# Kernel optimization log

Hardware: AMD Instinct MI355X
Metric: run time of the kernel (lower is better)

Reference implementation:

```python
import jax, jax.numpy as jnp
import numpy as np

K_REP = 4          # repulsion neighbors
REP_THRESH = 0.02  # repulsion distance threshold
K_NORM = 16        # PCA-normal neighborhood size (includes self)
CD_W, REP_W, NORM_W = 1.0, 0.1, 0.01


def _pdist2(x, y):
    # squared pairwise distances: [B,N,M]
    xx = (x * x).sum(-1)
    yy = (y * y).sum(-1)
    return xx[..., :, None] + yy[..., None, :] - 2.0 * jnp.einsum('bnd,bmd->bnm', x, y)


def _gather_points(pts, idx):
    # pts: [B,N,3], idx: [B,N,k] -> [B,N,k,3]
    return jax.vmap(lambda p, i: p[i])(pts, idx)


def _pca_normals(pts):
    # normals via PCA over K_NORM nearest neighbors (self included)
    D = _pdist2(pts, pts)                       # [B,N,N]
    _, idx = jax.lax.top_k(-D, K_NORM)          # [B,N,K]
    nb = _gather_points(pts, idx)               # [B,N,K,3]
    c = nb - nb.mean(axis=-2, keepdims=True)
    cov = jnp.einsum('bnkd,bnke->bnde', c, c) / K_NORM  # [B,N,3,3]
    _, vecs = jnp.linalg.eigh(cov)              # ascending eigenvalues
    return vecs[..., :, 0]                      # eigenvector of smallest eigenvalue


def reference(pred, gt):
    # --- chamfer distance (squared, bidirectional mean) ---
    Dpg = _pdist2(pred, gt)                     # [B,N,M]
    cd = Dpg.min(axis=-1).mean() + Dpg.min(axis=-2).mean()

    # --- repulsion loss: k=4 NN on pred (excluding self) ---
    Dpp = _pdist2(pred, pred)                   # [B,N,N]
    neg_d2, _ = jax.lax.top_k(-Dpp, K_REP + 1)  # nearest incl. self
    d2 = -neg_d2[..., 1:]                       # drop self
    d = jnp.sqrt(jnp.maximum(d2, 1e-12))
    rep = jax.nn.relu(REP_THRESH - d).mean()

    # --- normal consistency via PCA normals (k=16) ---
    n_pred = _pca_normals(pred)
    n_gt = _pca_normals(gt)
    normc = 1.0 - (n_pred * n_gt).sum(-1).mean()

    return CD_W * cd + REP_W * rep + NORM_W * normc


def setup_inputs() -> dict:
    key = jax.random.key(0)
    k1, k2 = jax.random.split(key)
    B, N = 8, 2048
    pred = jax.random.uniform(k1, (B, N, 3), dtype=jnp.float32)
    gt = jax.random.uniform(k2, (B, N, 3), dtype=jnp.float32)
    return {"pred": pred, "gt": gt}
```

## Files before the change

kernel.cpp:

```cpp
#include <hip/hip_runtime.h>


#define NB 8
#define NP 2048
#define KW 10
#define KN 16


__device__ __forceinline__ float f_slapy2(float x, float y) {
    float xa = fabsf(x), ya = fabsf(y);
    float w = fmaxf(xa, ya), zm = fminf(xa, ya);
    if (zm == 0.f) return w;
    float q = zm / w;
    return w * sqrtf(1.f + q * q);
}

__device__ __forceinline__ void f_slartg(float f, float g, float* cs, float* sn, float* r) {
    if (g == 0.f) { *cs = 1.f; *sn = 0.f; *r = f; }
    else if (f == 0.f) { *cs = 0.f; *sn = copysignf(1.f, g); *r = fabsf(g); }
    else {
        float d = sqrtf(__fadd_rn(__fmul_rn(f, f), __fmul_rn(g, g)));
        *cs = fabsf(f) / d;
        *r  = copysignf(d, f);
        *sn = g / *r;
    }
}

__device__ void f_slaev2(float a, float b, float c,
                         float* rt1, float* rt2, float* cs1, float* sn1) {
    float sm = a + c;
    float df = a - c;
    float adf = fabsf(df);
    float tb = b + b;
    float ab = fabsf(tb);
    float acmx, acmn;
    if (fabsf(a) > fabsf(c)) { acmx = a; acmn = c; } else { acmx = c; acmn = a; }
    float rt;
    if (adf > ab)      { float q = ab / adf; rt = adf * sqrtf(1.f + q * q); }
    else if (adf < ab) { float q = adf / ab; rt = ab * sqrtf(1.f + q * q); }
    else               rt = ab * sqrtf(2.f);
    int sgn1;
    if (sm < 0.f) {
        *rt1 = 0.5f * (sm - rt); sgn1 = -1;
        *rt2 = (acmx / *rt1) * acmn - (b / *rt1) * b;
    } else if (sm > 0.f) {
        *rt1 = 0.5f * (sm + rt); sgn1 = 1;
        *rt2 = (acmx / *rt1) * acmn - (b / *rt1) * b;
    } else {
        *rt1 = 0.5f * rt; *rt2 = -0.5f * rt; sgn1 = 1;
    }
    float cs; int sgn2;
    if (df >= 0.f) { cs = df + rt; sgn2 = 1; }
    else           { cs = df - rt; sgn2 = -1; }
    float acs = fabsf(cs);
    if (acs > ab) {
        float ct = -tb / cs;
        *sn1 = 1.f / sqrtf(1.f + ct * ct);
        *cs1 = ct * *sn1;
    } else {
        if (ab == 0.f) { *cs1 = 1.f; *sn1 = 0.f; }
        else {
            float tn = -cs / tb;
            *cs1 = 1.f / sqrtf(1.f + tn * tn);
            *sn1 = tn * *cs1;
        }
    }
    if (sgn1 == sgn2) { float tn = *cs1; *cs1 = -*sn1; *sn1 = tn; }
}


__device__ __forceinline__ float get3(float a, float b, float c, int i) {
    return i == 0 ? a : (i == 1 ? b : c);
}
__device__ __forceinline__ void set3(float& a, float& b, float& c, int i, float v) {
    a = (i == 0) ? v : a;
    b = (i == 1) ? v : b;
    c = (i == 2) ? v : c;
}
__device__ __forceinline__ float get2(float a, float b, int i) { return i == 0 ? a : b; }
__device__ __forceinline__ void set2(float& a, float& b, int i, float v) {
    a = (i == 0) ? v : a;
    b = (i == 1) ? v : b;
}

#define DGET(i)    get3(dd0, dd1, dd2, (i))
#define DSET(i, v) set3(dd0, dd1, dd2, (i), (v))
#define EGET(i)    get2(ee0, ee1, (i))
#define ESET(i, v) set2(ee0, ee1, (i), (v))
#define ZGET(r, c)    get3(z##r##0, z##r##1, z##r##2, (c))
#define ZSET(r, c, v) set3(z##r##0, z##r##1, z##r##2, (c), (v))
#define ZROT(r, ca, cb, cc, ss) { float zt_ = ZGET(r, (ca)); float zb_ = ZGET(r, (cb)); \
    ZSET(r, (ca), (cc) * zt_ - (ss) * zb_); ZSET(r, (cb), (ss) * zt_ + (cc) * zb_); }
#define ZROT3(ca, cb, cc, ss) { ZROT(0, (ca), (cb), (cc), (ss)) ZROT(1, (ca), (cb), (cc), (ss)) ZROT(2, (ca), (cb), (cc), (ss)) }

__device__ void ssyevd3_evec0(float a00, float a10, float a20,
                              float a11, float a21, float a22,
                              float* ox, float* oy, float* oz) {
    float dd0, dd1, dd2, ee0, ee1;
    float tau = 0.f, v2 = 0.f;
    float xnorm = fabsf(a20);
    if (xnorm == 0.f) {
        tau = 0.f;
        dd0 = a00; dd1 = a11; dd2 = a22; ee0 = a10; ee1 = a21;
    } else {
        float beta = -copysignf(f_slapy2(a10, xnorm), a10);
        tau = (beta - a10) / beta;
        float inv = 1.f / (a10 - beta);
        v2 = a20 * inv;
        float x1 = tau * (a11 + a21 * v2);
        float x2 = tau * (a21 + a22 * v2);
        float alpha = -0.5f * tau * (x1 + x2 * v2);
        float w1 = x1 + alpha;
        float w2 = x2 + alpha * v2;
        float b11 = a11 - 2.f * w1;
        float b21 = a21 - v2 * w1 - w2;
        float b22 = a22 - 2.f * (v2 * w2);
        dd0 = a00; dd1 = b11; dd2 = b22; ee0 = beta; ee1 = b21;
    }
    const float eps    = 5.9604645e-08f;
    const float eps2   = eps * eps;
    const float safmin = 1.1754944e-38f;
    const float ssfmax = sqrtf(1.f / safmin) / 3.f;
    const float ssfmin = sqrtf(safmin) / eps2;
    const int n = 3, nmaxit = 90;
    float z00 = 1.f, z01 = 0.f, z02 = 0.f;
    float z10 = 0.f, z11 = 1.f, z12 = 0.f;
    float z20 = 0.f, z21 = 0.f, z22 = 1.f;
    int jtot = 0;
    int l1 = 1;

    while (true) {
        if (l1 > n) break;
        if (l1 > 1) ESET(l1 - 2, 0.f);
        int m = n;
        {
            bool found = false;
            #pragma unroll
            for (int mi = 1; mi <= 2; ++mi) {
                if (!found && mi >= l1) {
                    float tst = fabsf(EGET(mi - 1));
                    if (tst == 0.f) { m = mi; found = true; }
                    else if (tst <= (sqrtf(fabsf(DGET(mi - 1))) * sqrtf(fabsf(DGET(mi)))) * eps) {
                        ESET(mi - 1, 0.f); m = mi; found = true;
                    }
                }
            }
        }
        int l = l1, lsv = l, lend = m, lendsv = lend;
        l1 = m + 1;
        if (lend == l) continue;

        float anorm = 0.f;
        #pragma unroll
        for (int i = 1; i <= 3; ++i)
            if (i >= l && i <= lend) anorm = fmaxf(anorm, fabsf(DGET(i - 1)));
        #pragma unroll
        for (int i = 1; i <= 2; ++i)
            if (i >= l && i <= lend - 1) anorm = fmaxf(anorm, fabsf(EGET(i - 1)));
        int iscale = 0; float sclto = 1.f;
        if (anorm == 0.f) continue;
        if (anorm > ssfmax) { iscale = 1; sclto = ssfmax; }
        else if (anorm < ssfmin) { iscale = 2; sclto = ssfmin; }
        if (iscale) {
            float mul = sclto / anorm;
            #pragma unroll
            for (int i = 1; i <= 3; ++i)
                if (i >= l && i <= lend) DSET(i - 1, DGET(i - 1) * mul);
            #pragma unroll
            for (int i = 1; i <= 2; ++i)
                if (i >= l && i <= lend - 1) ESET(i - 1, EGET(i - 1) * mul);
        }
        if (fabsf(DGET(lend - 1)) < fabsf(DGET(l - 1))) { lend = lsv; l = lendsv; }

        if (lend > l) {
            while (true) {
                int mq = lend;
                if (l != lend) {
                    bool found = false;
                    #pragma unroll
                    for (int i = 1; i <= 2; ++i) {
                        if (!found && i >= l && i <= lend - 1) {
                            float ei = EGET(i - 1);
                            float tst = ei * ei;
                            if (tst <= (eps2 * fabsf(DGET(i - 1))) * fabsf(DGET(i)) + safmin) { mq = i; found = true; }
                        }
                    }
                }
                if (mq < lend) ESET(mq - 1, 0.f);
                float p = DGET(l - 1);
                if (mq == l) { DSET(l - 1, p); l = l + 1; if (l <= lend) continue; break; }
                if (mq == l + 1) {
                    float rt1, rt2, c, s;
                    f_slaev2(DGET(l - 1), EGET(l - 1), DGET(l), &rt1, &rt2, &c, &s);
                    ZROT3(l, l - 1, c, s);
                    DSET(l - 1, rt1); DSET(l, rt2); ESET(l - 1, 0.f);
                    l += 2; if (l <= lend) continue; break;
                }
                if (jtot == nmaxit) break;
                jtot++;
                float g = (DGET(l) - p) / (2.f * EGET(l - 1));
                float r = f_slapy2(g, 1.f);
                g = DGET(mq - 1) - p + EGET(l - 1) / (g + copysignf(r, g));
                float s = 1.f, c = 1.f; p = 0.f;
                float cw0 = 0.f, cw1 = 0.f, sw0 = 0.f, sw1 = 0.f;
                #pragma unroll
                for (int i = 2; i >= 1; --i) {
                    if (i <= mq - 1 && i >= l) {
                        float f = s * EGET(i - 1);
                        float b = c * EGET(i - 1);
                        f_slartg(g, f, &c, &s, &r);
                        if (i != mq - 1) ESET(i, r);
                        g = DGET(i) - p;
                        r = (DGET(i - 1) - g) * s + 2.f * c * b;
                        p = s * r;
                        DSET(i, g + p);
                        g = c * r - b;
                        set2(cw0, cw1, i - l, c);
                        set2(sw0, sw1, i - l, -s);
                    }
                }
                #pragma unroll
                for (int j = 2; j >= 1; --j) {
                    if (j <= mq - l) {
                        float cj = get2(cw0, cw1, j - 1), sj = get2(sw0, sw1, j - 1);
                        int c0 = l - 1 + (j - 1);
                        ZROT3(c0 + 1, c0, cj, sj);
                    }
                }
                DSET(l - 1, DGET(l - 1) - p);
                ESET(l - 1, g);
            }
        } else {
            while (true) {
                int mq = lend;
                if (l != lend) {
                    bool found = false;
                    #pragma unroll
                    for (int i = 3; i >= 2; --i) {
                        if (!found && i <= l && i >= lend + 1) {
                            float ei = EGET(i - 2);
                            float tst = ei * ei;
                            if (tst <= (eps2 * fabsf(DGET(i - 1))) * fabsf(DGET(i - 2)) + safmin) { mq = i; found = true; }
                        }
                    }
                }
                if (mq > lend) ESET(mq - 2, 0.f);
                float p = DGET(l - 1);
                if (mq == l) { DSET(l - 1, p); l = l - 1; if (l >= lend) continue; break; }
                if (mq == l - 1) {
                    float rt1, rt2, c, s;
                    f_slaev2(DGET(l - 2), EGET(l - 2), DGET(l - 1), &rt1, &rt2, &c, &s);
                    ZROT3(l - 1, l - 2, c, s);
                    DSET(l - 2, rt1); DSET(l - 1, rt2); ESET(l - 2, 0.f);
                    l -= 2; if (l >= lend) continue; break;
                }
                if (jtot == nmaxit) break;
                jtot++;
                float g = (DGET(l - 2) - p) / (2.f * EGET(l - 2));
                float r = f_slapy2(g, 1.f);
                g = DGET(mq - 1) - p + EGET(l - 2) / (g + copysignf(r, g));
                float s = 1.f, c = 1.f; p = 0.f;
                float cw0 = 0.f, cw1 = 0.f, sw0 = 0.f, sw1 = 0.f;
                #pragma unroll
                for (int i = 1; i <= 2; ++i) {
                    if (i >= mq && i <= l - 1) {
                        float f = s * EGET(i - 1);
                        float b = c * EGET(i - 1);
                        f_slartg(g, f, &c, &s, &r);
                        if (i != mq) ESET(i - 2, r);
                        g = DGET(i - 1) - p;
                        r = (DGET(i) - g) * s + 2.f * c * b;
                        p = s * r;
                        DSET(i - 1, g + p);
                        g = c * r - b;
                        set2(cw0, cw1, i - mq, c);
                        set2(sw0, sw1, i - mq, s);
                    }
                }
                #pragma unroll
                for (int j = 1; j <= 2; ++j) {
                    if (j <= l - mq) {
                        float cj = get2(cw0, cw1, j - 1), sj = get2(sw0, sw1, j - 1);
                        int c0 = mq - 1 + (j - 1);
                        ZROT3(c0 + 1, c0, cj, sj);
                    }
                }
                DSET(l - 1, DGET(l - 1) - p);
                ESET(l - 2, g);
            }
        }
        if (iscale) {
            float mul = anorm / sclto;
            #pragma unroll
            for (int i = 1; i <= 3; ++i)
                if (i >= lsv && i <= lendsv) DSET(i - 1, DGET(i - 1) * mul);
            #pragma unroll
            for (int i = 1; i <= 2; ++i)
                if (i >= lsv && i <= lendsv - 1) ESET(i - 1, EGET(i - 1) * mul);
        }
        if (jtot >= nmaxit) break;
    }

    #pragma unroll
    for (int ii = 2; ii <= 3; ++ii) {
        int i = ii - 1, k = i;
        float p = DGET(i - 1);
        #pragma unroll
        for (int j = ii; j <= 3; ++j)
            if (DGET(j - 1) < p) { k = j; p = DGET(j - 1); }
        if (k != i) {
            DSET(k - 1, DGET(i - 1)); DSET(i - 1, p);
            { float t0 = ZGET(0, i - 1); ZSET(0, i - 1, ZGET(0, k - 1)); ZSET(0, k - 1, t0); }
            { float t1 = ZGET(1, i - 1); ZSET(1, i - 1, ZGET(1, k - 1)); ZSET(1, k - 1, t1); }
            { float t2 = ZGET(2, i - 1); ZSET(2, i - 1, ZGET(2, k - 1)); ZSET(2, k - 1, t2); }
        }
    }
    float r0 = z00, r1 = z10, r2 = z20;
    if (tau != 0.f) {
        float sum = r1 + v2 * r2;
        r1 -= tau * sum;
        r2 -= tau * (v2 * sum);
    }
    *ox = r0; *oy = r1; *oz = r2;
}


__device__ __forceinline__ float dot_rn(float ax, float ay, float az,
                                        float bx, float by, float bz) {
    return __fadd_rn(__fadd_rn(__fmul_rn(ax, bx), __fmul_rn(ay, by)), __fmul_rn(az, bz));
}

__device__ __forceinline__ void chain10(unsigned k[KW], unsigned x) {
    unsigned t = x;
    #pragma unroll
    for (int s = 0; s < KW; ++s) {
        unsigned lo = k[s] < t ? k[s] : t;
        unsigned hi = k[s] < t ? t : k[s];
        k[s] = lo; t = hi;
    }
}
__device__ __forceinline__ void chain16(unsigned k[KN], unsigned x) {
    unsigned t = x;
    #pragma unroll
    for (int s = 0; s < KN; ++s) {
        unsigned lo = k[s] < t ? k[s] : t;
        unsigned hi = k[s] < t ? t : k[s];
        k[s] = lo; t = hi;
    }
}

#define KIDX(s, w, l) (((s) * 8 + (w)) * 64 + (l))

__global__ __launch_bounds__(512, 4) void scan_kernel(
    const float* __restrict__ pred, const float* __restrict__ gt,
    float* __restrict__ nP, float* __restrict__ nG, double* __restrict__ acc)
{
    __shared__ float4 sHome[NP];
    __shared__ float4 sOther[NP];
    unsigned* kbuf = (unsigned*)sOther;
    float* mbuf = (float*)((char*)sOther + 20480);
    float* cache = (float*)sOther;

    int bi = blockIdx.x;
    bool predHome = bi < NB * 32;
    int lb = predHome ? bi : bi - NB * 32;
    int b = lb >> 5;
    int tile = lb & 31;
    int tid  = threadIdx.x;
    int wave = tid >> 6;
    int lane = tid & 63;

    const float* home  = (predHome ? pred : gt) + (size_t)b * NP * 3;
    const float* other = (predHome ? gt : pred) + (size_t)b * NP * 3;

    for (int t = tid; t < NP; t += 512) {
        float hx = home[3 * t], hy = home[3 * t + 1], hz = home[3 * t + 2];
        sHome[t] = make_float4(hx, hy, hz, dot_rn(hx, hy, hz, hx, hy, hz));
        float ox = other[3 * t], oy = other[3 * t + 1], oz = other[3 * t + 2];
        sOther[t] = make_float4(ox, oy, oz, 0.f);
    }
    __syncthreads();

    int im = tile * 64 + lane;
    float4 q = sHome[im];
    float qx = q.x, qy = q.y, qz = q.z, qq = q.w;

    unsigned keys[KW];
    #pragma unroll
    for (int s = 0; s < KW; ++s) keys[s] = 0x7F800000u | (unsigned)s;

    float minv = 1e30f;

    for (int t = 0; t < NP / 8; ++t) {
        int jj = (t << 3) | wave;
        float4 h = sHome[jj];
        float dotj = dot_rn(qx, qy, qz, h.x, h.y, h.z);
        float d2 = __fsub_rn(__fadd_rn(qq, h.w), __fmul_rn(2.f, dotj));
        chain10(keys, (__float_as_uint(d2) & 0xFFFFF800u) | (unsigned)jj);
        float4 o = sOther[jj];
        float ex = qx - o.x, ey = qy - o.y, ez = qz - o.z;
        minv = fminf(minv, fmaf(ex, ex, fmaf(ey, ey, ez * ez)));
    }
    __syncthreads();

    #pragma unroll
    for (int s = 0; s < KW; ++s) kbuf[KIDX(s, wave, lane)] = keys[s];
    mbuf[wave * 64 + lane] = minv;
    __syncthreads();

    if (wave != 0) return;

    unsigned k16[KN];
    #pragma unroll
    for (int s = 0; s < KW; ++s) k16[s] = keys[s];
    #pragma unroll
    for (int s = KW; s < KN; ++s) k16[s] = 0x7F800000u | (unsigned)s;
    for (int w = 1; w < 8; ++w) {
        #pragma unroll
        for (int s = 0; s < KW; ++s) chain16(k16, kbuf[KIDX(s, w, lane)]);
    }
    minv = fminf(fminf(fminf(mbuf[lane], mbuf[64 + lane]),
                       fminf(mbuf[128 + lane], mbuf[192 + lane])),
                 fminf(fminf(mbuf[256 + lane], mbuf[320 + lane]),
                       fminf(mbuf[384 + lane], mbuf[448 + lane])));

    unsigned flags = 0;
    #pragma unroll
    for (int w = 0; w < 8; ++w)
        flags |= (kbuf[KIDX(KW - 1, w, lane)] < k16[15]) ? (1u << w) : 0u;

    if (__any(flags != 0)) {
        #pragma unroll
        for (int s = 0; s < KN; ++s)
            k16[s] = flags ? (0x7F800000u | (unsigned)s) : k16[s];
        for (int w = 0; w < 8; ++w) {
            #pragma unroll
            for (int s = 0; s < KW; ++s) {
                unsigned kk = kbuf[KIDX(s, w, lane)];
                bool use = (flags != 0) && !((flags >> w) & 1);
                chain16(k16, use ? kk : 0xFFFFFFFFu);
            }
        }
        for (int w = 0; w < 8; ++w) {
            if (__any((flags >> w) & 1)) {
                bool actw = ((flags >> w) & 1) != 0;
                for (int t = 0; t < NP / 8; ++t) {
                    int jj = (t << 3) | w;
                    float4 h = sHome[jj];
                    float dotj = dot_rn(qx, qy, qz, h.x, h.y, h.z);
                    float d2 = __fsub_rn(__fadd_rn(qq, h.w), __fmul_rn(2.f, dotj));
                    unsigned key = (__float_as_uint(d2) & 0xFFFFF800u) | (unsigned)jj;
                    chain16(k16, actw ? key : 0xFFFFFFFFu);
                }
            }
        }
    }

    float rep = 0.0f;
    if (predHome) {
        #pragma unroll
        for (int r = 1; r <= 4; ++r) {
            float d2 = __uint_as_float(k16[r] & 0xFFFFF800u);
            float dd = sqrtf(fmaxf(d2, 1e-12f));
            rep += fmaxf(0.02f - dd, 0.0f);
        }
    }

    float sx = 0.f, sy = 0.f, sz = 0.f;
    #pragma unroll
    for (int s = 0; s < KN; ++s) {
        const float* hp = home + 3 * (size_t)(k16[s] & 0x7FFu);
        float px = hp[0], py = hp[1], pz = hp[2];
        cache[(s * 3 + 0) * 64 + lane] = px;
        cache[(s * 3 + 1) * 64 + lane] = py;
        cache[(s * 3 + 2) * 64 + lane] = pz;
        sx += px; sy += py; sz += pz;
    }
    float mx = sx * (1.0f / KN), my = sy * (1.0f / KN), mz = sz * (1.0f / KN);
    float cxx = 0.f, cxy = 0.f, cxz = 0.f, cyy = 0.f, cyz = 0.f, czz = 0.f;
    #pragma unroll
    for (int s = 0; s < KN; ++s) {
        float ax = cache[(s * 3 + 0) * 64 + lane] - mx;
        float ay = cache[(s * 3 + 1) * 64 + lane] - my;
        float az = cache[(s * 3 + 2) * 64 + lane] - mz;
        cxx += ax * ax; cxy += ax * ay; cxz += ax * az;
        cyy += ay * ay; cyz += ay * az; czz += az * az;
    }
    cxx *= (1.f / KN); cxy *= (1.f / KN); cxz *= (1.f / KN);
    cyy *= (1.f / KN); cyz *= (1.f / KN); czz *= (1.f / KN);

    float nx, ny, nz;
    ssyevd3_evec0(cxx, cxy, cxz, cyy, cyz, czz, &nx, &ny, &nz);

    float* nout = predHome ? nP : nG;
    int gi = b * NP + im;
    nout[gi * 3 + 0] = nx;
    nout[gi * 3 + 1] = ny;
    nout[gi * 3 + 2] = nz;

    double part = (double)minv * (1.0 / (NB * NP))
                + (double)rep  * (0.1 / (NB * NP * 4));

    #pragma unroll
    for (int off = 32; off > 0; off >>= 1) part += __shfl_down(part, off);
    if (lane == 0) atomicAdd(acc, part);
}

__global__ __launch_bounds__(64) void dot_kernel(
    const float* __restrict__ nP, const float* __restrict__ nG,
    double* __restrict__ acc)
{
    int vt = blockIdx.x * 64 + threadIdx.x;
    float s = 0.f;
    for (int i = vt; i < NB * NP; i += 1024)
        s += nP[3 * i] * nG[3 * i] + nP[3 * i + 1] * nG[3 * i + 1] + nP[3 * i + 2] * nG[3 * i + 2];
    double part = (double)s;
    #pragma unroll
    for (int off = 32; off > 0; off >>= 1) part += __shfl_down(part, off);
    if (threadIdx.x == 0) atomicAdd(acc + 1, part);
}

__global__ void fin_kernel(const double* __restrict__ acc, float* __restrict__ out)
{
    out[0] = (float)(acc[0] - acc[1] * (0.01 / (NB * NP)) + 0.01);
}

extern "C" void kernel_launch(void* const* d_in, const int* in_sizes, int n_in,
                              void* d_out, int out_size, void* d_ws, size_t ws_size,
                              hipStream_t stream)
{
    const float* pred = (const float*)d_in[0];
    const float* gt   = (const float*)d_in[1];

    char* base = (char*)d_ws;
    double* acc = (double*)base;
    float* nP = (float*)(base + 64);
    float* nG = nP + (size_t)NB * NP * 3;

    hipMemsetAsync(d_ws, 0, 64, stream);
    scan_kernel<<<dim3(NB * 32 * 2), dim3(512), 0, stream>>>(pred, gt, nP, nG, acc);
    dot_kernel<<<dim3(16), dim3(64), 0, stream>>>(nP, nG, acc);
    fin_kernel<<<dim3(1), dim3(1), 0, stream>>>(acc, (float*)d_out);
}
```

Before: 164.8 us.

## Split eigen-solve into separate kernel and gather neighbors from shared memory

The scan kernel now writes the six unique covariance entries per point to a workspace buffer, and a new small kernel runs the 3x3 symmetric eigen-solve separately. Neighbor coordinates for the PCA step are read from the shared sHome array instead of global memory plus a shared staging cache. The intent is to take register pressure and long serial code out of the heavy scan kernel, so it can keep more waves resident. The cost is one extra launch and a round-trip of the covariance data through global memory.

Result: no change. 164.9 us (+0.1%).

```diff
diff --git a/kernel.cpp b/kernel.cpp
--- a/kernel.cpp
+++ b/kernel.cpp
@@ -5,6 +5,7 @@
 #define NP 2048
 #define KW 10
 #define KN 16
+#define NQ (2 * NB * NP)
 
 
 __device__ __forceinline__ float f_slapy2(float x, float y) {
@@ -353,13 +354,12 @@
 
 __global__ __launch_bounds__(512, 4) void scan_kernel(
     const float* __restrict__ pred, const float* __restrict__ gt,
-    float* __restrict__ nP, float* __restrict__ nG, double* __restrict__ acc)
+    float* __restrict__ cov, double* __restrict__ acc)
 {
     __shared__ float4 sHome[NP];
     __shared__ float4 sOther[NP];
     unsigned* kbuf = (unsigned*)sOther;
     float* mbuf = (float*)((char*)sOther + 20480);
-    float* cache = (float*)sOther;
 
     int bi = blockIdx.x;
     bool predHome = bi < NB * 32;
@@ -469,34 +469,27 @@
     float sx = 0.f, sy = 0.f, sz = 0.f;
     #pragma unroll
     for (int s = 0; s < KN; ++s) {
-        const float* hp = home + 3 * (size_t)(k16[s] & 0x7FFu);
-        float px = hp[0], py = hp[1], pz = hp[2];
-        cache[(s * 3 + 0) * 64 + lane] = px;
-        cache[(s * 3 + 1) * 64 + lane] = py;
-        cache[(s * 3 + 2) * 64 + lane] = pz;
-        sx += px; sy += py; sz += pz;
+        float4 p = sHome[k16[s] & 0x7FFu];
+        sx += p.x; sy += p.y; sz += p.z;
     }
     float mx = sx * (1.0f / KN), my = sy * (1.0f / KN), mz = sz * (1.0f / KN);
     float cxx = 0.f, cxy = 0.f, cxz = 0.f, cyy = 0.f, cyz = 0.f, czz = 0.f;
     #pragma unroll
     for (int s = 0; s < KN; ++s) {
-        float ax = cache[(s * 3 + 0) * 64 + lane] - mx;
-        float ay = cache[(s * 3 + 1) * 64 + lane] - my;
-        float az = cache[(s * 3 + 2) * 64 + lane] - mz;
+        float4 p = sHome[k16[s] & 0x7FFu];
+        float ax = p.x - mx;
+        float ay = p.y - my;
+        float az = p.z - mz;
         cxx += ax * ax; cxy += ax * ay; cxz += ax * az;
         cyy += ay * ay; cyz += ay * az; czz += az * az;
     }
     cxx *= (1.f / KN); cxy *= (1.f / KN); cxz *= (1.f / KN);
     cyy *= (1.f / KN); cyz *= (1.f / KN); czz *= (1.f / KN);
 
-    float nx, ny, nz;
-    ssyevd3_evec0(cxx, cxy, cxz, cyy, cyz, czz, &nx, &ny, &nz);
-
-    float* nout = predHome ? nP : nG;
-    int gi = b * NP + im;
-    nout[gi * 3 + 0] = nx;
-    nout[gi * 3 + 1] = ny;
-    nout[gi * 3 + 2] = nz;
+    int gq = (predHome ? 0 : NB * NP) + b * NP + im;
+    float* cv = cov + (size_t)gq * 6;
+    cv[0] = cxx; cv[1] = cxy; cv[2] = cxz;
+    cv[3] = cyy; cv[4] = cyz; cv[5] = czz;
 
     double part = (double)minv * (1.0 / (NB * NP))
                 + (double)rep  * (0.1 / (NB * NP * 4));
@@ -504,6 +497,18 @@
     #pragma unroll
     for (int off = 32; off > 0; off >>= 1) part += __shfl_down(part, off);
     if (lane == 0) atomicAdd(acc, part);
+}
+
+__global__ __launch_bounds__(128) void eig_kernel(
+    const float* __restrict__ cov, float* __restrict__ nP, float* __restrict__ nG)
+{
+    int q = blockIdx.x * 128 + threadIdx.x;
+    if (q >= NQ) return;
+    const float* cv = cov + (size_t)q * 6;
+    float nx, ny, nz;
+    ssyevd3_evec0(cv[0], cv[1], cv[2], cv[3], cv[4], cv[5], &nx, &ny, &nz);
+    float* nout = (q < NB * NP) ? (nP + (size_t)q * 3) : (nG + (size_t)(q - NB * NP) * 3);
+    nout[0] = nx; nout[1] = ny; nout[2] = nz;
 }
 
 __global__ __launch_bounds__(64) void dot_kernel(
@@ -534,11 +539,13 @@
 
     char* base = (char*)d_ws;
     double* acc = (double*)base;
-    float* nP = (float*)(base + 64);
-    float* nG = nP + (size_t)NB * NP * 3;
+    float* nP  = (float*)(base + 64);
+    float* nG  = nP + (size_t)NB * NP * 3;
+    float* cov = nG + (size_t)NB * NP * 3;
 
     hipMemsetAsync(d_ws, 0, 64, stream);
-    scan_kernel<<<dim3(NB * 32 * 2), dim3(512), 0, stream>>>(pred, gt, nP, nG, acc);
+    scan_kernel<<<dim3(NB * 32 * 2), dim3(512), 0, stream>>>(pred, gt, cov, acc);
+    eig_kernel<<<dim3((NQ + 127) / 128), dim3(128), 0, stream>>>(cov, nP, nG);
     dot_kernel<<<dim3(16), dim3(64), 0, stream>>>(nP, nG, acc);
     fin_kernel<<<dim3(1), dim3(1), 0, stream>>>(acc, (float*)d_out);
 }
```

## Spread per-query merge and PCA across all waves, drop atomics and memset

Applied to the files above, without the earlier changes.

The post-scan merge of per-wave top-k lists, the fallback rescan, and the PCA normal step previously ran on wave 0 only, with 64 lanes per block. They now run on 8 lanes in each of the 8 waves. Neighbor coordinates are read from the shared sHome buffer instead of global memory. Global double atomics and the memset are replaced by per-block partial sums that a 512-thread final kernel reduces. The change uses more waves for the serial tail, but only 8 lanes per wave are active, so the fallback rescan may now be taken in more waves.

Result: slower. 195.5 us (+18.7%).

```diff
diff --git a/kernel.cpp b/kernel.cpp
--- a/kernel.cpp
+++ b/kernel.cpp
@@ -353,13 +353,14 @@
 
 __global__ __launch_bounds__(512, 4) void scan_kernel(
     const float* __restrict__ pred, const float* __restrict__ gt,
-    float* __restrict__ nP, float* __restrict__ nG, double* __restrict__ acc)
+    float* __restrict__ nP, float* __restrict__ nG,
+    double* __restrict__ cdpart)
 {
     __shared__ float4 sHome[NP];
     __shared__ float4 sOther[NP];
     unsigned* kbuf = (unsigned*)sOther;
     float* mbuf = (float*)((char*)sOther + 20480);
-    float* cache = (float*)sOther;
+    double* wsum = (double*)((char*)sOther + 22528);
 
     int bi = blockIdx.x;
     bool predHome = bi < NB * 32;
@@ -382,8 +383,8 @@
     __syncthreads();
 
     int im = tile * 64 + lane;
-    float4 q = sHome[im];
-    float qx = q.x, qy = q.y, qz = q.z, qq = q.w;
+    float4 qv = sHome[im];
+    float qx = qv.x, qy = qv.y, qz = qv.z, qq = qv.w;
 
     unsigned keys[KW];
     #pragma unroll
@@ -408,107 +409,117 @@
     mbuf[wave * 64 + lane] = minv;
     __syncthreads();
 
-    if (wave != 0) return;
-
-    unsigned k16[KN];
-    #pragma unroll
-    for (int s = 0; s < KW; ++s) k16[s] = keys[s];
-    #pragma unroll
-    for (int s = KW; s < KN; ++s) k16[s] = 0x7F800000u | (unsigned)s;
-    for (int w = 1; w < 8; ++w) {
-        #pragma unroll
-        for (int s = 0; s < KW; ++s) chain16(k16, kbuf[KIDX(s, w, lane)]);
-    }
-    minv = fminf(fminf(fminf(mbuf[lane], mbuf[64 + lane]),
-                       fminf(mbuf[128 + lane], mbuf[192 + lane])),
-                 fminf(fminf(mbuf[256 + lane], mbuf[320 + lane]),
-                       fminf(mbuf[384 + lane], mbuf[448 + lane])));
-
-    unsigned flags = 0;
-    #pragma unroll
-    for (int w = 0; w < 8; ++w)
-        flags |= (kbuf[KIDX(KW - 1, w, lane)] < k16[15]) ? (1u << w) : 0u;
-
-    if (__any(flags != 0)) {
-        #pragma unroll
-        for (int s = 0; s < KN; ++s)
-            k16[s] = flags ? (0x7F800000u | (unsigned)s) : k16[s];
-        for (int w = 0; w < 8; ++w) {
-            #pragma unroll
-            for (int s = 0; s < KW; ++s) {
-                unsigned kk = kbuf[KIDX(s, w, lane)];
-                bool use = (flags != 0) && !((flags >> w) & 1);
-                chain16(k16, use ? kk : 0xFFFFFFFFu);
+    double wavepart = 0.0;
+    if (lane < 8) {
+        int q = wave * 8 + lane;
+        int imq = tile * 64 + q;
+        float4 qp = sHome[imq];
+        float tqx = qp.x, tqy = qp.y, tqz = qp.z, tqq = qp.w;
+
+        unsigned k16[KN];
+        #pragma unroll
+        for (int s = 0; s < KW; ++s) k16[s] = kbuf[KIDX(s, 0, q)];
+        #pragma unroll
+        for (int s = KW; s < KN; ++s) k16[s] = 0x7F800000u | (unsigned)s;
+        for (int w = 1; w < 8; ++w) {
+            #pragma unroll
+            for (int s = 0; s < KW; ++s) chain16(k16, kbuf[KIDX(s, w, q)]);
+        }
+        float qminv = fminf(fminf(fminf(mbuf[q], mbuf[64 + q]),
+                                  fminf(mbuf[128 + q], mbuf[192 + q])),
+                            fminf(fminf(mbuf[256 + q], mbuf[320 + q]),
+                                  fminf(mbuf[384 + q], mbuf[448 + q])));
+
+        unsigned flags = 0;
+        #pragma unroll
+        for (int w = 0; w < 8; ++w)
+            flags |= (kbuf[KIDX(KW - 1, w, q)] < k16[15]) ? (1u << w) : 0u;
+
+        if (__any(flags != 0)) {
+            #pragma unroll
+            for (int s = 0; s < KN; ++s)
+                k16[s] = flags ? (0x7F800000u | (unsigned)s) : k16[s];
+            for (int w = 0; w < 8; ++w) {
+                #pragma unroll
+                for (int s = 0; s < KW; ++s) {
+                    unsigned kk = kbuf[KIDX(s, w, q)];
+                    bool use = (flags != 0) && !((flags >> w) & 1);
+                    chain16(k16, use ? kk : 0xFFFFFFFFu);
+                }
             }
-        }
-        for (int w = 0; w < 8; ++w) {
-            if (__any((flags >> w) & 1)) {
-                bool actw = ((flags >> w) & 1) != 0;
-                for (int t = 0; t < NP / 8; ++t) {
-                    int jj = (t << 3) | w;
-                    float4 h = sHome[jj];
-                    float dotj = dot_rn(qx, qy, qz, h.x, h.y, h.z);
-                    float d2 = __fsub_rn(__fadd_rn(qq, h.w), __fmul_rn(2.f, dotj));
-                    unsigned key = (__float_as_uint(d2) & 0xFFFFF800u) | (unsigned)jj;
-                    chain16(k16, actw ? key : 0xFFFFFFFFu);
+            for (int w = 0; w < 8; ++w) {
+                if (__any((flags >> w) & 1)) {
+                    bool actw = ((flags >> w) & 1) != 0;
+                    for (int t = 0; t < NP / 8; ++t) {
+                        int jj = (t << 3) | w;
+                        float4 h = sHome[jj];
+                        float dotj = dot_rn(tqx, tqy, tqz, h.x, h.y, h.z);
+                        float d2 = __fsub_rn(__fadd_rn(tqq, h.w), __fmul_rn(2.f, dotj));
+                        unsigned key = (__float_as_uint(d2) & 0xFFFFF800u) | (unsigned)jj;
+                        chain16(k16, actw ? key : 0xFFFFFFFFu);
+                    }
                 }
             }
         }
-    }
-
-    float rep = 0.0f;
-    if (predHome) {
-        #pragma unroll
-        for (int r = 1; r <= 4; ++r) {
-            float d2 = __uint_as_float(k16[r] & 0xFFFFF800u);
-            float dd = sqrtf(fmaxf(d2, 1e-12f));
-            rep += fmaxf(0.02f - dd, 0.0f);
-        }
-    }
-
-    float sx = 0.f, sy = 0.f, sz = 0.f;
-    #pragma unroll
-    for (int s = 0; s < KN; ++s) {
-        const float* hp = home + 3 * (size_t)(k16[s] & 0x7FFu);
-        float px = hp[0], py = hp[1], pz = hp[2];
-        cache[(s * 3 + 0) * 64 + lane] = px;
-        cache[(s * 3 + 1) * 64 + lane] = py;
-        cache[(s * 3 + 2) * 64 + lane] = pz;
-        sx += px; sy += py; sz += pz;
-    }
-    float mx = sx * (1.0f / KN), my = sy * (1.0f / KN), mz = sz * (1.0f / KN);
-    float cxx = 0.f, cxy = 0.f, cxz = 0.f, cyy = 0.f, cyz = 0.f, czz = 0.f;
-    #pragma unroll
-    for (int s = 0; s < KN; ++s) {
-        float ax = cache[(s * 3 + 0) * 64 + lane] - mx;
-        float ay = cache[(s * 3 + 1) * 64 + lane] - my;
-        float az = cache[(s * 3 + 2) * 64 + lane] - mz;
-        cxx += ax * ax; cxy += ax * ay; cxz += ax * az;
-        cyy += ay * ay; cyz += ay * az; czz += az * az;
-    }
-    cxx *= (1.f / KN); cxy *= (1.f / KN); cxz *= (1.f / KN);
-    cyy *= (1.f / KN); cyz *= (1.f / KN); czz *= (1.f / KN);
-
-    float nx, ny, nz;
-    ssyevd3_evec0(cxx, cxy, cxz, cyy, cyz, czz, &nx, &ny, &nz);
-
-    float* nout = predHome ? nP : nG;
-    int gi = b * NP + im;
-    nout[gi * 3 + 0] = nx;
-    nout[gi * 3 + 1] = ny;
-    nout[gi * 3 + 2] = nz;
-
-    double part = (double)minv * (1.0 / (NB * NP))
-                + (double)rep  * (0.1 / (NB * NP * 4));
-
-    #pragma unroll
-    for (int off = 32; off > 0; off >>= 1) part += __shfl_down(part, off);
-    if (lane == 0) atomicAdd(acc, part);
+
+        float rep = 0.0f;
+        if (predHome) {
+            #pragma unroll
+            for (int r = 1; r <= 4; ++r) {
+                float d2 = __uint_as_float(k16[r] & 0xFFFFF800u);
+                float dd = sqrtf(fmaxf(d2, 1e-12f));
+                rep += fmaxf(0.02f - dd, 0.0f);
+            }
+        }
+
+        float sx = 0.f, sy = 0.f, sz = 0.f;
+        #pragma unroll
+        for (int s = 0; s < KN; ++s) {
+            float4 p = sHome[k16[s] & 0x7FFu];
+            sx += p.x; sy += p.y; sz += p.z;
+        }
+        float mx = sx * (1.0f / KN), my = sy * (1.0f / KN), mz = sz * (1.0f / KN);
+        float cxx = 0.f, cxy = 0.f, cxz = 0.f, cyy = 0.f, cyz = 0.f, czz = 0.f;
+        #pragma unroll
+        for (int s = 0; s < KN; ++s) {
+            float4 p = sHome[k16[s] & 0x7FFu];
+            float ax = p.x - mx;
+            float ay = p.y - my;
+            float az = p.z - mz;
+            cxx += ax * ax; cxy += ax * ay; cxz += ax * az;
+            cyy += ay * ay; cyz += ay * az; czz += az * az;
+        }
+        cxx *= (1.f / KN); cxy *= (1.f / KN); cxz *= (1.f / KN);
+        cyy *= (1.f / KN); cyz *= (1.f / KN); czz *= (1.f / KN);
+
+        float nx, ny, nz;
+        ssyevd3_evec0(cxx, cxy, cxz, cyy, cyz, czz, &nx, &ny, &nz);
+
+        float* nout = predHome ? nP : nG;
+        int gi = b * NP + imq;
+        nout[gi * 3 + 0] = nx;
+        nout[gi * 3 + 1] = ny;
+        nout[gi * 3 + 2] = nz;
+
+        wavepart = (double)qminv * (1.0 / (NB * NP))
+                 + (double)rep   * (0.1 / (NB * NP * 4));
+    }
+
+    #pragma unroll
+    for (int off = 4; off > 0; off >>= 1) wavepart += __shfl_down(wavepart, off);
+    if (lane == 0) wsum[wave] = wavepart;
+    __syncthreads();
+    if (tid == 0) {
+        double t = 0.0;
+        #pragma unroll
+        for (int w = 0; w < 8; ++w) t += wsum[w];
+        cdpart[bi] = t;
+    }
 }
 
 __global__ __launch_bounds__(64) void dot_kernel(
     const float* __restrict__ nP, const float* __restrict__ nG,
-    double* __restrict__ acc)
+    double* __restrict__ dotpart)
 {
     int vt = blockIdx.x * 64 + threadIdx.x;
     float s = 0.f;
@@ -517,12 +528,31 @@
     double part = (double)s;
     #pragma unroll
     for (int off = 32; off > 0; off >>= 1) part += __shfl_down(part, off);
-    if (threadIdx.x == 0) atomicAdd(acc + 1, part);
-}
-
-__global__ void fin_kernel(const double* __restrict__ acc, float* __restrict__ out)
+    if (threadIdx.x == 0) dotpart[blockIdx.x] = part;
+}
+
+__global__ __launch_bounds__(512) void fin_kernel(
+    const double* __restrict__ cdpart, const double* __restrict__ dotpart,
+    float* __restrict__ out)
 {
-    out[0] = (float)(acc[0] - acc[1] * (0.01 / (NB * NP)) + 0.01);
+    __shared__ double wc[8], wd[8];
+    int tid = threadIdx.x;
+    int wave = tid >> 6, lane = tid & 63;
+    double c = cdpart[tid];
+    double d = (tid < 16) ? dotpart[tid] : 0.0;
+    #pragma unroll
+    for (int off = 32; off > 0; off >>= 1) {
+        c += __shfl_down(c, off);
+        d += __shfl_down(d, off);
+    }
+    if (lane == 0) { wc[wave] = c; wd[wave] = d; }
+    __syncthreads();
+    if (tid == 0) {
+        double a = 0.0, t = 0.0;
+        #pragma unroll
+        for (int w = 0; w < 8; ++w) { a += wc[w]; t += wd[w]; }
+        out[0] = (float)(a - t * (0.01 / (NB * NP)) + 0.01);
+    }
 }
 
 extern "C" void kernel_launch(void* const* d_in, const int* in_sizes, int n_in,
@@ -533,12 +563,12 @@
     const float* gt   = (const float*)d_in[1];
 
     char* base = (char*)d_ws;
-    double* acc = (double*)base;
-    float* nP = (float*)(base + 64);
-    float* nG = nP + (size_t)NB * NP * 3;
-
-    hipMemsetAsync(d_ws, 0, 64, stream);
-    scan_kernel<<<dim3(NB * 32 * 2), dim3(512), 0, stream>>>(pred, gt, nP, nG, acc);
-    dot_kernel<<<dim3(16), dim3(64), 0, stream>>>(nP, nG, acc);
-    fin_kernel<<<dim3(1), dim3(1), 0, stream>>>(acc, (float*)d_out);
-}
+    float*  nP      = (float*)base;
+    float*  nG      = nP + (size_t)NB * NP * 3;
+    double* cdpart  = (double*)(nG + (size_t)NB * NP * 3);
+    double* dotpart = cdpart + 512;
+
+    scan_kernel<<<dim3(NB * 32 * 2), dim3(512), 0, stream>>>(pred, gt, nP, nG, cdpart);
+    dot_kernel<<<dim3(16), dim3(64), 0, stream>>>(nP, nG, dotpart);
+    fin_kernel<<<dim3(1), dim3(512), 0, stream>>>(cdpart, dotpart, (float*)d_out);
+}
```

## Merge dot and final kernels, drop memset and atomics, read neighbors from LDS

Applied to the files above, without the earlier changes.

Per-block partial sums are now written to a workspace array instead of being accumulated with double atomics, so the memset is no longer needed. The separate dot and final kernels are merged into one 1024-thread reduction kernel, which cuts launches from four operations to two. PCA neighbor coordinates are read from the shared home array instead of global memory plus a shared cache. This reduces launch and serialization overhead and global gathers, but the final reduction now runs in a single block.

New measurement: 162.3 us. No clear change (-1.5%).

```diff
diff --git a/kernel.cpp b/kernel.cpp
--- a/kernel.cpp
+++ b/kernel.cpp
@@ -353,13 +353,13 @@
 
 __global__ __launch_bounds__(512, 4) void scan_kernel(
     const float* __restrict__ pred, const float* __restrict__ gt,
-    float* __restrict__ nP, float* __restrict__ nG, double* __restrict__ acc)
+    float* __restrict__ nP, float* __restrict__ nG,
+    double* __restrict__ cdpart)
 {
     __shared__ float4 sHome[NP];
     __shared__ float4 sOther[NP];
     unsigned* kbuf = (unsigned*)sOther;
     float* mbuf = (float*)((char*)sOther + 20480);
-    float* cache = (float*)sOther;
 
     int bi = blockIdx.x;
     bool predHome = bi < NB * 32;
@@ -382,8 +382,8 @@
     __syncthreads();
 
     int im = tile * 64 + lane;
-    float4 q = sHome[im];
-    float qx = q.x, qy = q.y, qz = q.z, qq = q.w;
+    float4 qv = sHome[im];
+    float qx = qv.x, qy = qv.y, qz = qv.z, qq = qv.w;
 
     unsigned keys[KW];
     #pragma unroll
@@ -469,20 +469,17 @@
     float sx = 0.f, sy = 0.f, sz = 0.f;
     #pragma unroll
     for (int s = 0; s < KN; ++s) {
-        const float* hp = home + 3 * (size_t)(k16[s] & 0x7FFu);
-        float px = hp[0], py = hp[1], pz = hp[2];
-        cache[(s * 3 + 0) * 64 + lane] = px;
-        cache[(s * 3 + 1) * 64 + lane] = py;
-        cache[(s * 3 + 2) * 64 + lane] = pz;
-        sx += px; sy += py; sz += pz;
+        float4 p = sHome[k16[s] & 0x7FFu];
+        sx += p.x; sy += p.y; sz += p.z;
     }
     float mx = sx * (1.0f / KN), my = sy * (1.0f / KN), mz = sz * (1.0f / KN);
     float cxx = 0.f, cxy = 0.f, cxz = 0.f, cyy = 0.f, cyz = 0.f, czz = 0.f;
     #pragma unroll
     for (int s = 0; s < KN; ++s) {
-        float ax = cache[(s * 3 + 0) * 64 + lane] - mx;
-        float ay = cache[(s * 3 + 1) * 64 + lane] - my;
-        float az = cache[(s * 3 + 2) * 64 + lane] - mz;
+        float4 p = sHome[k16[s] & 0x7FFu];
+        float ax = p.x - mx;
+        float ay = p.y - my;
+        float az = p.z - mz;
         cxx += ax * ax; cxy += ax * ay; cxz += ax * az;
         cyy += ay * ay; cyz += ay * az; czz += az * az;
     }
@@ -503,26 +500,37 @@
 
     #pragma unroll
     for (int off = 32; off > 0; off >>= 1) part += __shfl_down(part, off);
-    if (lane == 0) atomicAdd(acc, part);
-}
-
-__global__ __launch_bounds__(64) void dot_kernel(
+    if (lane == 0) cdpart[bi] = part;
+}
+
+__global__ __launch_bounds__(1024) void fin_kernel(
     const float* __restrict__ nP, const float* __restrict__ nG,
-    double* __restrict__ acc)
+    const double* __restrict__ cdpart, float* __restrict__ out)
 {
-    int vt = blockIdx.x * 64 + threadIdx.x;
+    __shared__ double wc[16], wd[16];
+    int tid = threadIdx.x;
+    int wave = tid >> 6, lane = tid & 63;
+
     float s = 0.f;
-    for (int i = vt; i < NB * NP; i += 1024)
+    for (int i = tid; i < NB * NP; i += 1024)
         s += nP[3 * i] * nG[3 * i] + nP[3 * i + 1] * nG[3 * i + 1] + nP[3 * i + 2] * nG[3 * i + 2];
-    double part = (double)s;
-    #pragma unroll
-    for (int off = 32; off > 0; off >>= 1) part += __shfl_down(part, off);
-    if (threadIdx.x == 0) atomicAdd(acc + 1, part);
-}
-
-__global__ void fin_kernel(const double* __restrict__ acc, float* __restrict__ out)
-{
-    out[0] = (float)(acc[0] - acc[1] * (0.01 / (NB * NP)) + 0.01);
+    double d = (double)s;
+
+    double c = (tid < 512) ? cdpart[tid] : 0.0;
+
+    #pragma unroll
+    for (int off = 32; off > 0; off >>= 1) {
+        c += __shfl_down(c, off);
+        d += __shfl_down(d, off);
+    }
+    if (lane == 0) { wc[wave] = c; wd[wave] = d; }
+    __syncthreads();
+    if (tid == 0) {
+        double a = 0.0, t = 0.0;
+        #pragma unroll
+        for (int w = 0; w < 16; ++w) { a += wc[w]; t += wd[w]; }
+        out[0] = (float)(a - t * (0.01 / (NB * NP)) + 0.01);
+    }
 }
 
 extern "C" void kernel_launch(void* const* d_in, const int* in_sizes, int n_in,
@@ -533,12 +541,10 @@
     const float* gt   = (const float*)d_in[1];
 
     char* base = (char*)d_ws;
-    double* acc = (double*)base;
-    float* nP = (float*)(base + 64);
-    float* nG = nP + (size_t)NB * NP * 3;
-
-    hipMemsetAsync(d_ws, 0, 64, stream);
-    scan_kernel<<<dim3(NB * 32 * 2), dim3(512), 0, stream>>>(pred, gt, nP, nG, acc);
-    dot_kernel<<<dim3(16), dim3(64), 0, stream>>>(nP, nG, acc);
-    fin_kernel<<<dim3(1), dim3(1), 0, stream>>>(acc, (float*)d_out);
-}
+    float*  nP     = (float*)base;
+    float*  nG     = nP + (size_t)NB * NP * 3;
+    double* cdpart = (double*)(nG + (size_t)NB * NP * 3);
+
+    scan_kernel<<<dim3(NB * 32 * 2), dim3(512), 0, stream>>>(pred, gt, nP, nG, cdpart);
+    fin_kernel<<<dim3(1), dim3(1024), 0, stream>>>(nP, nG, cdpart, (float*)d_out);
+}
```
